# Kernel tuning notes

Measured on AMD Instinct MI355X. Metric: run time of the kernel, lower is better.

## Reference

```python
import jax, jax.numpy as jnp
import numpy as np

B, N, C, H = 16, 1024, 768, 12
D = C // H          # head dim = 64
HID = 4 * C         # 3072
EPS = 1e-5


def layernorm(x, g, b):
    m = x.mean(-1, keepdims=True)
    v = ((x - m) ** 2).mean(-1, keepdims=True)
    return (x - m) * jax.lax.rsqrt(v + EPS) * g + b


def setup_inputs() -> dict:
    key = jax.random.key(0)
    ks = jax.random.split(key, 10)
    s = 0.02
    return {
        "x": jax.random.normal(ks[0], (B, N, C), dtype=jnp.float32),
        "ln1_g": jnp.ones((C,), jnp.float32), "ln1_b": jnp.zeros((C,), jnp.float32),
        "wq": jax.random.normal(ks[1], (C, C)) * s, "bq": jnp.zeros((C,), jnp.float32),
        "wk": jax.random.normal(ks[2], (C, C)) * s, "bk": jnp.zeros((C,), jnp.float32),
        "wv": jax.random.normal(ks[3], (C, C)) * s, "bv": jnp.zeros((C,), jnp.float32),
        "wp": jax.random.normal(ks[4], (C, C)) * s, "bp": jnp.zeros((C,), jnp.float32),
        "ln2_g": jnp.ones((C,), jnp.float32), "ln2_b": jnp.zeros((C,), jnp.float32),
        "w1": jax.random.normal(ks[5], (HID, C)) * s, "b1": jnp.zeros((HID,), jnp.float32),
        "w2": jax.random.normal(ks[6], (C, HID)) * s, "b2": jnp.zeros((C,), jnp.float32),
        "gate_h": jax.random.normal(ks[7], (H,), dtype=jnp.float32),
        "gate_f": jax.random.normal(ks[8], (HID,), dtype=jnp.float32),
    }


def reference(x, ln1_g, ln1_b, wq, bq, wk, bk, wv, bv, wp, bp,
              ln2_g, ln2_b, w1, b1, w2, b2, gate_h, gate_f):
    # steady-state path: k_dynamic=None, is_warmup=False -> dyn gates are all ones,
    # so head_mask / ffn_mask reduce to the hard static gates (STE is identity on ones).
    head_mask = (jax.nn.sigmoid(gate_h) > 0.5).astype(x.dtype)            # [H]
    hm = jnp.broadcast_to(head_mask, (B, H))                              # [B,H]

    # --- attention branch ---
    xn = layernorm(x, ln1_g, ln1_b)
    split = lambda t: t.reshape(B, N, H, D).transpose(0, 2, 1, 3)          # [B,H,N,D]
    q = split(xn @ wq.T + bq)
    k = split(xn @ wk.T + bk)
    v = split(xn @ wv.T + bv)
    scale = D ** -0.5
    attn = jax.nn.softmax(jnp.einsum('bhqd,bhkd->bhqk', q, k) * scale, axis=-1)
    y = jnp.einsum('bhqk,bhkd->bhqd', attn, v)
    y = y * hm[:, :, None, None]                                           # per-head mask on y
    xa = y.transpose(0, 2, 1, 3).reshape(B, N, C)
    hm_flat = jnp.repeat(hm, D, axis=-1).reshape(B, 1, C)                  # mask applied a 2nd time
    xa = (xa * hm_flat) @ wp.T + bp
    x = x + xa

    # --- gated MLP branch ---
    fmask = (jax.nn.sigmoid(gate_f) > 0.5).astype(x.dtype)[None, None, :]  # [1,1,HID]
    xn2 = layernorm(x, ln2_g, ln2_b)
    f1 = xn2 @ w1.T + b1
    f1 = jax.nn.gelu(f1 * fmask, approximate=False) * fmask                # mask -> GELU -> mask
    x = x + f1 @ w2.T + b2
    return x
```

## Files before the change

kernel.cpp:

```cpp
#include <hip/hip_runtime.h>

#define BB 16
#define NNN 1024
#define CC 768
#define HH 12
#define DD 64
#define HIDN 3072
#define ROWS (BB*NNN)

typedef _Float16 half8 __attribute__((ext_vector_type(8)));
typedef _Float16 half4 __attribute__((ext_vector_type(4)));
typedef float floatx4 __attribute__((ext_vector_type(4)));

#define GLOAD_LDS(g, l) __builtin_amdgcn_global_load_lds( \
    (const __attribute__((address_space(1))) void*)(g),    \
    (__attribute__((address_space(3))) void*)(l), 16, 0, 0)

#define RAW_BARRIER() do { asm volatile("" ::: "memory"); \
    __builtin_amdgcn_s_barrier(); asm volatile("" ::: "memory"); } while (0)
#define VMCNT_WAIT(n) __builtin_amdgcn_s_waitcnt((n) | 0x0F70)

__global__ void cvt_kernel(const float* __restrict__ src, _Float16* __restrict__ dst, int n4) {
    int i = blockIdx.x * blockDim.x + threadIdx.x;
    if (i < n4) {
        floatx4 v = ((const floatx4*)src)[i];
        half4 h;
        h[0] = (_Float16)v[0]; h[1] = (_Float16)v[1];
        h[2] = (_Float16)v[2]; h[3] = (_Float16)v[3];
        ((half4*)dst)[i] = h;
    }
}

__global__ __launch_bounds__(256) void scan_kernel(const float* __restrict__ gf,
                                                   const float* __restrict__ b1,
                                                   int* __restrict__ meta,
                                                   int* __restrict__ perm,
                                                   float* __restrict__ b1c) {
    int t = threadIdx.x;
    int base = t * 12;
    bool act[12];
    int cnt = 0;
    #pragma unroll
    for (int i = 0; i < 12; i++) { bool a = gf[base + i] > 0.0f; act[i] = a; cnt += a ? 1 : 0; }
    __shared__ int cs[256];
    cs[t] = cnt;
    __syncthreads();
    if (t == 0) {
        int s = 0;
        for (int i = 0; i < 256; i++) { int c = cs[i]; cs[i] = s; s += c; }
        meta[1] = s;
        meta[0] = (s + 127) & ~127;
    }
    __syncthreads();
    int off = cs[t];
    for (int i = t; i < HIDN; i += 256) { b1c[i] = 0.0f; perm[i] = -1; }
    __syncthreads();
    #pragma unroll
    for (int i = 0; i < 12; i++)
        if (act[i]) { perm[off] = base + i; b1c[off] = b1[base + i]; off++; }
}

__global__ void gatherW1_kernel(const float* __restrict__ src, const int* __restrict__ perm,
                                _Float16* __restrict__ dst) {
    int i = blockIdx.x * blockDim.x + threadIdx.x;
    int row = i / 192, c4 = i - row * 192;
    int s = perm[row];
    half4 h; h[0] = h[1] = h[2] = h[3] = (_Float16)0.0f;
    if (s >= 0) {
        floatx4 v = ((const floatx4*)(src + (size_t)s * CC))[c4];
        h[0] = (_Float16)v[0]; h[1] = (_Float16)v[1];
        h[2] = (_Float16)v[2]; h[3] = (_Float16)v[3];
    }
    ((half4*)dst)[i] = h;
}

__global__ void gatherW2_kernel(const float* __restrict__ src, const int* __restrict__ perm,
                                _Float16* __restrict__ dst) {
    int i = blockIdx.x * blockDim.x + threadIdx.x;
    int n = i / 768, j4 = (i - n * 768) * 4;
    const float* r = src + (size_t)n * HIDN;
    half4 h;
    #pragma unroll
    for (int e = 0; e < 4; e++) {
        int s = perm[j4 + e];
        h[e] = (s >= 0) ? (_Float16)r[s] : (_Float16)0.0f;
    }
    *(half4*)&dst[(size_t)n * HIDN + j4] = h;
}

__global__ __launch_bounds__(256) void ln_kernel(const float* __restrict__ x,
                                                 const float* __restrict__ g,
                                                 const float* __restrict__ b,
                                                 _Float16* __restrict__ out) {
    int row = blockIdx.x;
    int t = threadIdx.x;
    const float* xr = x + (size_t)row * CC;
    float v0 = xr[t], v1 = xr[t + 256], v2 = xr[t + 512];
    float s = v0 + v1 + v2;
    float q = v0 * v0 + v1 * v1 + v2 * v2;
    #pragma unroll
    for (int m = 1; m < 64; m <<= 1) {
        s += __shfl_xor(s, m, 64);
        q += __shfl_xor(q, m, 64);
    }
    __shared__ float red[8];
    int wv = t >> 6, lane = t & 63;
    if (lane == 0) { red[wv] = s; red[wv + 4] = q; }
    __syncthreads();
    s = red[0] + red[1] + red[2] + red[3];
    q = red[4] + red[5] + red[6] + red[7];
    float mean = s * (1.0f / CC);
    float var = q * (1.0f / CC) - mean * mean;
    float rs = rsqrtf(var + 1e-5f);
    _Float16* orow = out + (size_t)row * CC;
    orow[t]       = (_Float16)((v0 - mean) * rs * g[t]       + b[t]);
    orow[t + 256] = (_Float16)((v1 - mean) * rs * g[t + 256] + b[t + 256]);
    orow[t + 512] = (_Float16)((v2 - mean) * rs * g[t + 512] + b[t + 512]);
}

template <int MODE, int TM>
__global__ __launch_bounds__(256) void gemm_kernel(
    const _Float16* __restrict__ A,
    const _Float16* __restrict__ W,
    const float* __restrict__ bias0,
    const float* __restrict__ bias1,
    const float* __restrict__ bias2,
    const float* __restrict__ res,
    const float* __restrict__ gate,
    const float* __restrict__ hgate,
    void* __restrict__ out0,
    void* __restrict__ out1,
    void* __restrict__ out2,
    const int* __restrict__ meta,
    int M, int N, int K)
{
    constexpr int MI = TM / 32;
    constexpr int AISS = TM / 32;
    constexpr int BISS = 4;
    constexpr int NISS = AISS + BISS;
    int GN = N >> 7, GM = M / TM;
    int f = blockIdx.x;
    int xcd = f & 7, slot = f >> 3;
    int m_idx = xcd * (GM >> 3) + slot / GN;
    int n_idx = slot - (slot / GN) * GN;
    int m0 = m_idx * TM, n0 = n_idx * 128;

    int Klen = K;
    if (meta) {
        if (MODE == 1) { if (n0 >= meta[0]) return; }
        if (MODE == 2) Klen = meta[0];
    }

    int seg = 0;
    if (MODE == 0) {
        seg = n0 / 768;
        int segc0 = n0 - seg * 768;
        int h0 = segc0 >> 6;
        if (hgate[h0] <= 0.0f && hgate[h0 + 1] <= 0.0f) return;
    }
    unsigned kmask = 0xFFFFFFFFu;
    if (MODE == 2 && hgate) {
        kmask = 0;
        for (int i = 0; i < HH; i++) kmask |= (hgate[i] > 0.0f ? 1u : 0u) << i;
    }

    __shared__ _Float16 As[2][TM * 64];
    __shared__ _Float16 Bs[2][128 * 64];
    int t = threadIdx.x;
    int lane = t & 63, w = t >> 6;
    int wm = (w >> 1) * (TM / 2), wn = (w & 1) * 64;
    int L = lane & 15, quad = lane >> 4;

    floatx4 acc[MI][4];
    #pragma unroll
    for (int i = 0; i < MI; i++)
        #pragma unroll
        for (int j = 0; j < 4; j++)
            acc[i][j] = (floatx4){0.f, 0.f, 0.f, 0.f};

    const _Float16* agp[AISS];
    const _Float16* bgp[BISS];
    #pragma unroll
    for (int i = 0; i < AISS; i++) {
        int pc = i * 256 + t;
        int row = pc >> 3;
        int kc = (pc & 7) ^ (row & 7);
        agp[i] = A + (size_t)(m0 + row) * K + kc * 8;
    }
    #pragma unroll
    for (int i = 0; i < BISS; i++) {
        int pc = i * 256 + t;
        int row = pc >> 3;
        int kc = (pc & 7) ^ (row & 7);
        bgp[i] = W + (size_t)(n0 + row) * K + kc * 8;
    }
    unsigned wb = (unsigned)w * 512;

    auto nextk = [&](int k0) -> int {
        if (MODE == 2)
            while (k0 < Klen && !((kmask >> ((k0 >> 6) & 31)) & 1)) k0 += 64;
        return k0;
    };
    auto stage = [&](int buf, int k0) {
        #pragma unroll
        for (int i = 0; i < AISS; i++) GLOAD_LDS(agp[i] + k0, &As[buf][i * 2048 + wb]);
        #pragma unroll
        for (int i = 0; i < BISS; i++) GLOAD_LDS(bgp[i] + k0, &Bs[buf][i * 2048 + wb]);
    };
    auto compute = [&](int buf) {
        #pragma unroll
        for (int kk = 0; kk < 2; kk++) {
            half8 af[MI], bf[4];
            #pragma unroll
            for (int i = 0; i < MI; i++)
                af[i] = *(const half8*)&As[buf][(wm + i * 16 + L) * 64 + ((kk * 4 + quad) ^ (L & 7)) * 8];
            #pragma unroll
            for (int j = 0; j < 4; j++)
                bf[j] = *(const half8*)&Bs[buf][(wn + j * 16 + L) * 64 + ((kk * 4 + quad) ^ (L & 7)) * 8];
            #pragma unroll
            for (int i = 0; i < MI; i++)
                #pragma unroll
                for (int j = 0; j < 4; j++)
                    acc[i][j] = __builtin_amdgcn_mfma_f32_16x16x32_f16(af[i], bf[j], acc[i][j], 0, 0, 0);
        }
    };

    int kcur = nextk(0);
    if (kcur < Klen) {
        stage(0, kcur);
        int kn1 = nextk(kcur + 64);
        int kn2 = Klen;
        if (kn1 < Klen) { stage(1, kn1); kn2 = nextk(kn1 + 64); }
        int buf = 0;
        while (kn2 < Klen) {
            VMCNT_WAIT(NISS);
            RAW_BARRIER();
            compute(buf);
            RAW_BARRIER();
            stage(buf, kn2);
            buf ^= 1;
            kn1 = kn2; kn2 = nextk(kn2 + 64);
        }
        if (kn1 < Klen) {
            VMCNT_WAIT(NISS);
            RAW_BARRIER();
            compute(buf);
            buf ^= 1;
        }
        VMCNT_WAIT(0);
        RAW_BARRIER();
        compute(buf);
    }

    #pragma unroll
    for (int i = 0; i < MI; i++) {
        #pragma unroll
        for (int j = 0; j < 4; j++) {
            int gn = n0 + wn + j * 16 + L;
            if (MODE == 0) {
                int col = gn - seg * 768;
                const float* bsel = (seg == 0) ? bias0 : (seg == 1) ? bias1 : bias2;
                float bs = bsel[col];
                if (seg < 2) {
                    _Float16* o = (_Float16*)((seg == 0) ? out0 : out1);
                    #pragma unroll
                    for (int r = 0; r < 4; r++) {
                        int gm = m0 + wm + i * 16 + quad * 4 + r;
                        o[(size_t)gm * CC + col] = (_Float16)(acc[i][j][r] + bs);
                    }
                } else {
                    int gm0 = m0 + wm + i * 16 + quad * 4;
                    int b_ = gm0 >> 10, n_ = gm0 & 1023;
                    half4 pk;
                    #pragma unroll
                    for (int r = 0; r < 4; r++) pk[r] = (_Float16)(acc[i][j][r] + bs);
                    size_t idx = ((size_t)(b_ * HH + (col >> 6)) * 64 + (col & 63)) * NNN + n_;
                    *(half4*)&((_Float16*)out2)[idx] = pk;
                }
            } else {
                float bs = bias0[gn];
                #pragma unroll
                for (int r = 0; r < 4; r++) {
                    int gm = m0 + wm + i * 16 + quad * 4 + r;
                    float v = acc[i][j][r] + bs;
                    size_t idx = (size_t)gm * N + gn;
                    if (MODE == 1) {
                        float vv = 0.5f * v * (1.0f + erff(v * 0.70710678118f));
                        if (gate && !(gate[gn] > 0.0f)) vv = 0.0f;
                        ((_Float16*)out0)[idx] = (_Float16)vv;
                    } else {
                        ((float*)out0)[idx] = res[idx] + v;
                    }
                }
            }
        }
    }
}

__global__ __launch_bounds__(256) void attn_kernel(
    const _Float16* __restrict__ Q,
    const _Float16* __restrict__ Kp,
    const _Float16* __restrict__ Vt,
    const float* __restrict__ gate_h,
    _Float16* __restrict__ Y)
{
    int qt = blockIdx.x;
    int h  = blockIdx.y;
    int b  = blockIdx.z;
    int t = threadIdx.x;
    int q0 = qt * 64;
    size_t ybase = ((size_t)b * NNN + q0) * CC + h * DD;

    if (gate_h[h] <= 0.0f) {
        int r = t >> 2, c = (t & 3) * 16;
        half8 z = {(_Float16)0, (_Float16)0, (_Float16)0, (_Float16)0,
                   (_Float16)0, (_Float16)0, (_Float16)0, (_Float16)0};
        *(half8*)&Y[ybase + (size_t)r * CC + c]     = z;
        *(half8*)&Y[ybase + (size_t)r * CC + c + 8] = z;
        return;
    }

    __shared__ _Float16 Qs[64][72];
    __shared__ _Float16 Ks[64][72];
    __shared__ _Float16 Vs[64][72];
    __shared__ _Float16 Ps[64][72];

    int lane = t & 63, w = t >> 6;
    int L = lane & 15, quad = lane >> 4;

    {
        int r = t >> 2, c = (t & 3) * 16;
        const half8* src = (const half8*)(Q + ((size_t)b * NNN + q0 + r) * CC + h * DD + c);
        half8 h0 = src[0], h1 = src[1];
        #pragma unroll
        for (int e = 0; e < 8; e++) { h0[e] = h0[e] * (_Float16)0.125f; h1[e] = h1[e] * (_Float16)0.125f; }
        *(half8*)&Qs[r][c]     = h0;
        *(half8*)&Qs[r][c + 8] = h1;
    }

    floatx4 O[4];
    float m_[4], l_[4];
    #pragma unroll
    for (int i = 0; i < 4; i++) { O[i] = (floatx4){0.f,0.f,0.f,0.f}; m_[i] = -1e30f; l_[i] = 0.0f; }

    const size_t kbase = (size_t)b * NNN * CC + h * DD;
    const size_t vbase = (size_t)(b * HH + h) * DD * NNN;

    for (int kt = 0; kt < 16; ++kt) {
        int k0 = kt * 64;
        __syncthreads();
        {
            int r = t >> 2, c = (t & 3) * 16;
            const half8* ks = (const half8*)(Kp + kbase + (size_t)(k0 + r) * CC + c);
            half8 ka = ks[0], kb = ks[1];
            *(half8*)&Ks[r][c]     = ka;
            *(half8*)&Ks[r][c + 8] = kb;
            const half8* vs = (const half8*)(Vt + vbase + (size_t)r * NNN + k0 + c);
            half8 va = vs[0], vb = vs[1];
            *(half8*)&Vs[r][c]     = va;
            *(half8*)&Vs[r][c + 8] = vb;
        }
        __syncthreads();

        half8 aq0 = *(const half8*)&Qs[16 * w + L][quad * 8];
        half8 aq1 = *(const half8*)&Qs[16 * w + L][quad * 8 + 32];
        floatx4 s[4];
        #pragma unroll
        for (int j = 0; j < 4; j++) {
            half8 b0 = *(const half8*)&Ks[16 * j + L][quad * 8];
            half8 b1 = *(const half8*)&Ks[16 * j + L][quad * 8 + 32];
            floatx4 z = (floatx4){0.f,0.f,0.f,0.f};
            z = __builtin_amdgcn_mfma_f32_16x16x32_f16(aq0, b0, z, 0, 0, 0);
            z = __builtin_amdgcn_mfma_f32_16x16x32_f16(aq1, b1, z, 0, 0, 0);
            s[j] = z;
        }

        #pragma unroll
        for (int r = 0; r < 4; r++) {
            float mx = fmaxf(fmaxf(s[0][r], s[1][r]), fmaxf(s[2][r], s[3][r]));
            mx = fmaxf(mx, __shfl_xor(mx, 1, 64));
            mx = fmaxf(mx, __shfl_xor(mx, 2, 64));
            mx = fmaxf(mx, __shfl_xor(mx, 4, 64));
            mx = fmaxf(mx, __shfl_xor(mx, 8, 64));
            float mnew = fmaxf(m_[r], mx);
            float alpha = __expf(m_[r] - mnew);
            m_[r] = mnew;
            float ps = 0.0f;
            #pragma unroll
            for (int j = 0; j < 4; j++) {
                float p = __expf(s[j][r] - mnew);
                s[j][r] = p; ps += p;
                Ps[16 * w + quad * 4 + r][L + 16 * j] = (_Float16)p;
            }
            ps += __shfl_xor(ps, 1, 64);
            ps += __shfl_xor(ps, 2, 64);
            ps += __shfl_xor(ps, 4, 64);
            ps += __shfl_xor(ps, 8, 64);
            l_[r] = l_[r] * alpha + ps;
            #pragma unroll
            for (int t4 = 0; t4 < 4; t4++) O[t4][r] *= alpha;
        }
        __syncthreads();

        half8 ap0 = *(const half8*)&Ps[16 * w + L][quad * 8];
        half8 ap1 = *(const half8*)&Ps[16 * w + L][quad * 8 + 32];
        #pragma unroll
        for (int t4 = 0; t4 < 4; t4++) {
            half8 b0 = *(const half8*)&Vs[16 * t4 + L][quad * 8];
            half8 b1 = *(const half8*)&Vs[16 * t4 + L][quad * 8 + 32];
            O[t4] = __builtin_amdgcn_mfma_f32_16x16x32_f16(ap0, b0, O[t4], 0, 0, 0);
            O[t4] = __builtin_amdgcn_mfma_f32_16x16x32_f16(ap1, b1, O[t4], 0, 0, 0);
        }
    }

    __syncthreads();
    #pragma unroll
    for (int r = 0; r < 4; r++) {
        float inv = 1.0f / l_[r];
        #pragma unroll
        for (int t4 = 0; t4 < 4; t4++)
            Ps[16 * w + quad * 4 + r][16 * t4 + L] = (_Float16)(O[t4][r] * inv);
    }
    __syncthreads();
    {
        int r = t >> 2, c = (t & 3) * 16;
        half8 o0 = *(const half8*)&Ps[r][c];
        half8 o1 = *(const half8*)&Ps[r][c + 8];
        *(half8*)&Y[ybase + (size_t)r * CC + c]     = o0;
        *(half8*)&Y[ybase + (size_t)r * CC + c + 8] = o1;
    }
}

extern "C" void kernel_launch(void* const* d_in, const int* in_sizes, int n_in,
                              void* d_out, int out_size, void* d_ws, size_t ws_size,
                              hipStream_t stream)
{
    const float* x      = (const float*)d_in[0];
    const float* ln1_g  = (const float*)d_in[1];
    const float* ln1_b  = (const float*)d_in[2];
    const float* wq     = (const float*)d_in[3];
    const float* bq     = (const float*)d_in[4];
    const float* wk     = (const float*)d_in[5];
    const float* bk     = (const float*)d_in[6];
    const float* wv     = (const float*)d_in[7];
    const float* bv     = (const float*)d_in[8];
    const float* wp     = (const float*)d_in[9];
    const float* bp     = (const float*)d_in[10];
    const float* ln2_g  = (const float*)d_in[11];
    const float* ln2_b  = (const float*)d_in[12];
    const float* w1     = (const float*)d_in[13];
    const float* b1     = (const float*)d_in[14];
    const float* w2     = (const float*)d_in[15];
    const float* b2     = (const float*)d_in[16];
    const float* gate_h = (const float*)d_in[17];
    const float* gate_f = (const float*)d_in[18];

    char* ws = (char*)d_ws;
    _Float16* WQKVh = (_Float16*)(ws + 0);
    _Float16* WPh = (_Float16*)(ws + 3538944);
    _Float16* W1c = (_Float16*)(ws + 4718592);
    _Float16* W2c = (_Float16*)(ws + 9437184);
    _Float16* XN  = (_Float16*)(ws + 14155776);
    _Float16* Qb  = (_Float16*)(ws + 39321600);
    _Float16* Kb  = (_Float16*)(ws + 64487424);
    _Float16* Vtb = (_Float16*)(ws + 89653248);
    _Float16* Yb  = (_Float16*)(ws + 114819072);
    float*    X1  = (float*)   (ws + 139984896);
    _Float16* XN2 = (_Float16*)(ws + 114819072);
    _Float16* F1  = (_Float16*)(ws + 14155776);
    int*      meta = (int*)    (ws + 190316544);
    int*      perm = (int*)    (ws + 190316800);
    float*    b1c  = (float*)  (ws + 190329088);

    scan_kernel<<<1, 256, 0, stream>>>(gate_f, b1, meta, perm, b1c);

    cvt_kernel<<<576, 256, 0, stream>>>(wq, WQKVh, 147456);
    cvt_kernel<<<576, 256, 0, stream>>>(wk, WQKVh + 589824, 147456);
    cvt_kernel<<<576, 256, 0, stream>>>(wv, WQKVh + 1179648, 147456);
    cvt_kernel<<<576, 256, 0, stream>>>(wp, WPh, 147456);
    gatherW1_kernel<<<2304, 256, 0, stream>>>(w1, perm, W1c);
    gatherW2_kernel<<<2304, 256, 0, stream>>>(w2, perm, W2c);

    ln_kernel<<<ROWS, 256, 0, stream>>>(x, ln1_g, ln1_b, XN);

    gemm_kernel<0, 128><<<2304, 256, 0, stream>>>(
        XN, WQKVh, bq, bk, bv, nullptr, nullptr, gate_h, Qb, Kb, Vtb, nullptr, ROWS, 2304, CC);

    attn_kernel<<<dim3(16, HH, BB), 256, 0, stream>>>(Qb, Kb, Vtb, gate_h, Yb);

    gemm_kernel<2, 64><<<1536, 256, 0, stream>>>(
        Yb, WPh, bp, nullptr, nullptr, x, nullptr, gate_h, X1, nullptr, nullptr, nullptr, ROWS, CC, CC);

    ln_kernel<<<ROWS, 256, 0, stream>>>(X1, ln2_g, ln2_b, XN2);

    gemm_kernel<1, 128><<<3072, 256, 0, stream>>>(
        XN2, W1c, b1c, nullptr, nullptr, nullptr, nullptr, nullptr, F1, nullptr, nullptr, meta, ROWS, HIDN, CC);

    gemm_kernel<2, 64><<<1536, 256, 0, stream>>>(
        F1, W2c, b2, nullptr, nullptr, X1, nullptr, nullptr, (float*)d_out, nullptr, nullptr, meta, ROWS, CC, HIDN);
}
```

Baseline: 465.3 us.

## Rewrite GEMM as 256x128 tile, 8-wave, triple-buffered interleaved load/MFMA pipeline

Replaces the templated double-buffered GEMM with a single 256x128 tile run by 512 threads (8 waves). It uses three LDS buffers and splits each K-tile into four phases, interleaving global-to-LDS loads for tile k+2 between MFMA bursts with setprio and sched barriers. The aim is to hide memory latency better and raise MFMA utilisation through larger tiles and finer-grained overlap. The cost is more LDS (about 144KB), fewer blocks for the small-N projection GEMMs (384 blocks), and many more barriers per K step.

Result: slower. 518.1 us (+11.3%).

```diff
diff --git a/kernel.cpp b/kernel.cpp
--- a/kernel.cpp
+++ b/kernel.cpp
@@ -19,6 +19,8 @@
 #define RAW_BARRIER() do { asm volatile("" ::: "memory"); \
     __builtin_amdgcn_s_barrier(); asm volatile("" ::: "memory"); } while (0)
 #define VMCNT_WAIT(n) __builtin_amdgcn_s_waitcnt((n) | 0x0F70)
+#define SCHED0() __builtin_amdgcn_sched_barrier(0)
+#define MFMA16(acc_, a_, b_) acc_ = __builtin_amdgcn_mfma_f32_16x16x32_f16(a_, b_, acc_, 0, 0, 0)
 
 __global__ void cvt_kernel(const float* __restrict__ src, _Float16* __restrict__ dst, int n4) {
     int i = blockIdx.x * blockDim.x + threadIdx.x;
@@ -118,8 +120,8 @@
     orow[t + 512] = (_Float16)((v2 - mean) * rs * g[t + 512] + b[t + 512]);
 }
 
-template <int MODE, int TM>
-__global__ __launch_bounds__(256) void gemm_kernel(
+template <int MODE>
+__global__ __launch_bounds__(512) void gemm_kernel(
     const _Float16* __restrict__ A,
     const _Float16* __restrict__ W,
     const float* __restrict__ bias0,
@@ -134,16 +136,12 @@
     const int* __restrict__ meta,
     int M, int N, int K)
 {
-    constexpr int MI = TM / 32;
-    constexpr int AISS = TM / 32;
-    constexpr int BISS = 4;
-    constexpr int NISS = AISS + BISS;
-    int GN = N >> 7, GM = M / TM;
+    int GN = N >> 7, GM = M >> 8;
     int f = blockIdx.x;
     int xcd = f & 7, slot = f >> 3;
     int m_idx = xcd * (GM >> 3) + slot / GN;
     int n_idx = slot - (slot / GN) * GN;
-    int m0 = m_idx * TM, n0 = n_idx * 128;
+    int m0 = m_idx * 256, n0 = n_idx * 128;
 
     int Klen = K;
     if (meta) {
@@ -164,96 +162,135 @@
         for (int i = 0; i < HH; i++) kmask |= (hgate[i] > 0.0f ? 1u : 0u) << i;
     }
 
-    __shared__ _Float16 As[2][TM * 64];
-    __shared__ _Float16 Bs[2][128 * 64];
+    __shared__ _Float16 As[3][256 * 64];
+    __shared__ _Float16 Bs[3][128 * 64];
     int t = threadIdx.x;
     int lane = t & 63, w = t >> 6;
-    int wm = (w >> 1) * (TM / 2), wn = (w & 1) * 64;
+    int wm = (w >> 1) * 64, wn = (w & 1) * 64;
     int L = lane & 15, quad = lane >> 4;
 
-    floatx4 acc[MI][4];
-    #pragma unroll
-    for (int i = 0; i < MI; i++)
+    floatx4 acc[4][4];
+    #pragma unroll
+    for (int i = 0; i < 4; i++)
         #pragma unroll
         for (int j = 0; j < 4; j++)
             acc[i][j] = (floatx4){0.f, 0.f, 0.f, 0.f};
 
-    const _Float16* agp[AISS];
-    const _Float16* bgp[BISS];
-    #pragma unroll
-    for (int i = 0; i < AISS; i++) {
-        int pc = i * 256 + t;
+    const _Float16* agp[4];
+    const _Float16* bgp[2];
+    #pragma unroll
+    for (int i = 0; i < 4; i++) {
+        int pc = i * 512 + t;
         int row = pc >> 3;
         int kc = (pc & 7) ^ (row & 7);
         agp[i] = A + (size_t)(m0 + row) * K + kc * 8;
     }
     #pragma unroll
-    for (int i = 0; i < BISS; i++) {
-        int pc = i * 256 + t;
+    for (int i = 0; i < 2; i++) {
+        int pc = i * 512 + t;
         int row = pc >> 3;
         int kc = (pc & 7) ^ (row & 7);
         bgp[i] = W + (size_t)(n0 + row) * K + kc * 8;
     }
-    unsigned wb = (unsigned)w * 512;
 
     auto nextk = [&](int k0) -> int {
         if (MODE == 2)
             while (k0 < Klen && !((kmask >> ((k0 >> 6) & 31)) & 1)) k0 += 64;
         return k0;
     };
-    auto stage = [&](int buf, int k0) {
-        #pragma unroll
-        for (int i = 0; i < AISS; i++) GLOAD_LDS(agp[i] + k0, &As[buf][i * 2048 + wb]);
-        #pragma unroll
-        for (int i = 0; i < BISS; i++) GLOAD_LDS(bgp[i] + k0, &Bs[buf][i * 2048 + wb]);
+    auto stage_full = [&](int buf, int k0) {
+        #pragma unroll
+        for (int i = 0; i < 4; i++) GLOAD_LDS(agp[i] + k0, &As[buf][i * 4096 + t * 8]);
+        #pragma unroll
+        for (int i = 0; i < 2; i++) GLOAD_LDS(bgp[i] + k0, &Bs[buf][i * 4096 + t * 8]);
     };
-    auto compute = [&](int buf) {
-        #pragma unroll
-        for (int kk = 0; kk < 2; kk++) {
-            half8 af[MI], bf[4];
-            #pragma unroll
-            for (int i = 0; i < MI; i++)
-                af[i] = *(const half8*)&As[buf][(wm + i * 16 + L) * 64 + ((kk * 4 + quad) ^ (L & 7)) * 8];
-            #pragma unroll
-            for (int j = 0; j < 4; j++)
-                bf[j] = *(const half8*)&Bs[buf][(wn + j * 16 + L) * 64 + ((kk * 4 + quad) ^ (L & 7)) * 8];
-            #pragma unroll
-            for (int i = 0; i < MI; i++)
-                #pragma unroll
-                for (int j = 0; j < 4; j++)
-                    acc[i][j] = __builtin_amdgcn_mfma_f32_16x16x32_f16(af[i], bf[j], acc[i][j], 0, 0, 0);
-        }
+    auto ldA = [&](int bi, int mi, int c) -> half8 {
+        int row = wm + mi * 16 + L;
+        return *(const half8*)&As[bi][row * 64 + (c ^ (L & 7)) * 8];
     };
-
-    int kcur = nextk(0);
-    if (kcur < Klen) {
-        stage(0, kcur);
-        int kn1 = nextk(kcur + 64);
-        int kn2 = Klen;
-        if (kn1 < Klen) { stage(1, kn1); kn2 = nextk(kn1 + 64); }
-        int buf = 0;
-        while (kn2 < Klen) {
-            VMCNT_WAIT(NISS);
-            RAW_BARRIER();
-            compute(buf);
-            RAW_BARRIER();
-            stage(buf, kn2);
-            buf ^= 1;
-            kn1 = kn2; kn2 = nextk(kn2 + 64);
-        }
-        if (kn1 < Klen) {
-            VMCNT_WAIT(NISS);
-            RAW_BARRIER();
-            compute(buf);
-            buf ^= 1;
-        }
-        VMCNT_WAIT(0);
+    auto ldB = [&](int bi, int nj, int c) -> half8 {
+        int row = wn + nj * 16 + L;
+        return *(const half8*)&Bs[bi][row * 64 + (c ^ (L & 7)) * 8];
+    };
+
+    auto run_tile = [&](int bi, bool more, int sbuf, int k2) {
+        half8 a0 = ldA(bi, 0, quad), a1 = ldA(bi, 1, quad);
+        half8 b0 = ldB(bi, 0, quad), b1 = ldB(bi, 1, quad);
+        half8 b2 = ldB(bi, 2, quad), b3 = ldB(bi, 3, quad);
+        if (more) { GLOAD_LDS(agp[0] + k2, &As[sbuf][t * 8]);
+                    GLOAD_LDS(agp[1] + k2, &As[sbuf][4096 + t * 8]); }
+        RAW_BARRIER(); SCHED0();
+        __builtin_amdgcn_s_setprio(1);
+        MFMA16(acc[0][0], a0, b0); MFMA16(acc[0][1], a0, b1);
+        MFMA16(acc[0][2], a0, b2); MFMA16(acc[0][3], a0, b3);
+        MFMA16(acc[1][0], a1, b0); MFMA16(acc[1][1], a1, b1);
+        MFMA16(acc[1][2], a1, b2); MFMA16(acc[1][3], a1, b3);
+        __builtin_amdgcn_s_setprio(0); SCHED0();
         RAW_BARRIER();
-        compute(buf);
-    }
-
-    #pragma unroll
-    for (int i = 0; i < MI; i++) {
+        half8 a2 = ldA(bi, 2, quad), a3 = ldA(bi, 3, quad);
+        if (more) { GLOAD_LDS(agp[2] + k2, &As[sbuf][8192 + t * 8]);
+                    GLOAD_LDS(agp[3] + k2, &As[sbuf][12288 + t * 8]); }
+        RAW_BARRIER(); SCHED0();
+        __builtin_amdgcn_s_setprio(1);
+        MFMA16(acc[2][0], a2, b0); MFMA16(acc[2][1], a2, b1);
+        MFMA16(acc[2][2], a2, b2); MFMA16(acc[2][3], a2, b3);
+        MFMA16(acc[3][0], a3, b0); MFMA16(acc[3][1], a3, b1);
+        MFMA16(acc[3][2], a3, b2); MFMA16(acc[3][3], a3, b3);
+        __builtin_amdgcn_s_setprio(0); SCHED0();
+        RAW_BARRIER();
+        a0 = ldA(bi, 0, 4 + quad); a1 = ldA(bi, 1, 4 + quad);
+        b0 = ldB(bi, 0, 4 + quad); b1 = ldB(bi, 1, 4 + quad);
+        b2 = ldB(bi, 2, 4 + quad); b3 = ldB(bi, 3, 4 + quad);
+        if (more) { GLOAD_LDS(bgp[0] + k2, &Bs[sbuf][t * 8]);
+                    GLOAD_LDS(bgp[1] + k2, &Bs[sbuf][4096 + t * 8]); }
+        RAW_BARRIER(); SCHED0();
+        __builtin_amdgcn_s_setprio(1);
+        MFMA16(acc[0][0], a0, b0); MFMA16(acc[0][1], a0, b1);
+        MFMA16(acc[0][2], a0, b2); MFMA16(acc[0][3], a0, b3);
+        MFMA16(acc[1][0], a1, b0); MFMA16(acc[1][1], a1, b1);
+        MFMA16(acc[1][2], a1, b2); MFMA16(acc[1][3], a1, b3);
+        __builtin_amdgcn_s_setprio(0); SCHED0();
+        RAW_BARRIER();
+        a2 = ldA(bi, 2, 4 + quad); a3 = ldA(bi, 3, 4 + quad);
+        if (more) { VMCNT_WAIT(6); } else { VMCNT_WAIT(0); }
+        RAW_BARRIER(); SCHED0();
+        __builtin_amdgcn_s_setprio(1);
+        MFMA16(acc[2][0], a2, b0); MFMA16(acc[2][1], a2, b1);
+        MFMA16(acc[2][2], a2, b2); MFMA16(acc[2][3], a2, b3);
+        MFMA16(acc[3][0], a3, b0); MFMA16(acc[3][1], a3, b1);
+        MFMA16(acc[3][2], a3, b2); MFMA16(acc[3][3], a3, b3);
+        __builtin_amdgcn_s_setprio(0); SCHED0();
+        RAW_BARRIER();
+    };
+
+    int kq0 = nextk(0);
+    if (kq0 < Klen) {
+        int kq1 = nextk(kq0 + 64);
+        stage_full(0, kq0);
+        int kq2;
+        if (kq1 < Klen) {
+            stage_full(1, kq1); kq2 = nextk(kq1 + 64);
+            VMCNT_WAIT(6);
+        } else {
+            kq2 = Klen;
+            VMCNT_WAIT(0);
+        }
+        RAW_BARRIER();
+        int bi = 0;
+        while (true) {
+            bool more = kq2 < Klen;
+            int sbuf = bi + 2; if (sbuf >= 3) sbuf -= 3;
+            run_tile(bi, more, sbuf, kq2);
+            kq0 = kq1;
+            if (kq0 >= Klen) break;
+            kq1 = kq2;
+            kq2 = more ? nextk(kq2 + 64) : Klen;
+            bi = bi + 1; if (bi >= 3) bi -= 3;
+        }
+    }
+
+    #pragma unroll
+    for (int i = 0; i < 4; i++) {
         #pragma unroll
         for (int j = 0; j < 4; j++) {
             int gn = n0 + wn + j * 16 + L;
@@ -483,19 +520,19 @@
 
     ln_kernel<<<ROWS, 256, 0, stream>>>(x, ln1_g, ln1_b, XN);
 
-    gemm_kernel<0, 128><<<2304, 256, 0, stream>>>(
+    gemm_kernel<0><<<1152, 512, 0, stream>>>(
         XN, WQKVh, bq, bk, bv, nullptr, nullptr, gate_h, Qb, Kb, Vtb, nullptr, ROWS, 2304, CC);
 
     attn_kernel<<<dim3(16, HH, BB), 256, 0, stream>>>(Qb, Kb, Vtb, gate_h, Yb);
 
-    gemm_kernel<2, 64><<<1536, 256, 0, stream>>>(
+    gemm_kernel<2><<<384, 512, 0, stream>>>(
         Yb, WPh, bp, nullptr, nullptr, x, nullptr, gate_h, X1, nullptr, nullptr, nullptr, ROWS, CC, CC);
 
     ln_kernel<<<ROWS, 256, 0, stream>>>(X1, ln2_g, ln2_b, XN2);
 
-    gemm_kernel<1, 128><<<3072, 256, 0, stream>>>(
+    gemm_kernel<1><<<1536, 512, 0, stream>>>(
         XN2, W1c, b1c, nullptr, nullptr, nullptr, nullptr, nullptr, F1, nullptr, nullptr, meta, ROWS, HIDN, CC);
 
-    gemm_kernel<2, 64><<<1536, 256, 0, stream>>>(
+    gemm_kernel<2><<<384, 512, 0, stream>>>(
         F1, W2c, b2, nullptr, nullptr, X1, nullptr, nullptr, (float*)d_out, nullptr, nullptr, meta, ROWS, CC, HIDN);
 }
```
